# Kernel optimization log

Measured on AMD Instinct MI355X. Metric: run time of the kernel, lower is better.

The kernel has to match this reference:

```python
import jax, jax.numpy as jnp
import numpy as np

B, T, E, H, L = 16, 512, 768, 12, 100
D = E // H
LN_EPS = 1e-12
NEG = -1e9


def setup_inputs() -> dict:
    key = jax.random.key(0)
    ks = jax.random.split(key, 12)
    s = 1.0 / np.sqrt(E)
    inp = {
        "last_hidden_states": jax.random.normal(ks[0], (B, T, E), jnp.float32),
        "att_mask": jnp.ones((B, T), jnp.float32),
        "type_emb": jax.random.normal(ks[1], (L, E), jnp.float32),
        # learned params
        "tp": jax.random.normal(ks[2], (E,), jnp.float32),
        "Wq": jax.random.normal(ks[3], (E, E), jnp.float32) * s,
        "bq": jnp.zeros((E,), jnp.float32),
        "Wk": jax.random.normal(ks[4], (E, E), jnp.float32) * s,
        "bk": jnp.zeros((E,), jnp.float32),
        "Wv": jax.random.normal(ks[5], (E, E), jnp.float32) * s,
        "bv": jnp.zeros((E,), jnp.float32),
        "Wo": jax.random.normal(ks[6], (E, E), jnp.float32) * s,
        "bo": jnp.zeros((E,), jnp.float32),
        "ln_g": jnp.ones((E,), jnp.float32),
        "ln_b": jnp.zeros((E,), jnp.float32),
    }
    return inp


def _layer_norm(x, g, b):
    mu = x.mean(-1, keepdims=True)
    var = ((x - mu) ** 2).mean(-1, keepdims=True)
    return (x - mu) * jax.lax.rsqrt(var + LN_EPS) * g + b


def reference(last_hidden_states, att_mask, type_emb, tp,
              Wq, bq, Wk, bk, Wv, bv, Wo, bo, ln_g, ln_b):
    b, t, e = last_hidden_states.shape
    # --- label cross-attention (no head split, no scaling) ---
    scores = jnp.einsum('bte,le->btl', last_hidden_states, type_emb)      # [b,t,l]
    att = jax.nn.softmax(scores, axis=-1)
    first_label_emb = jnp.einsum('btl,le->bte', att, type_emb)            # [b,t,e]

    h_truth = last_hidden_states + first_label_emb
    h_unknown = last_hidden_states + tp                                   # broadcast tp over [b,t]

    # --- two-stream masked self-attention: Q from unknown, K/V from truth,
    #     each position masked from attending to its own truth state ---
    q = (h_unknown @ Wq + bq).reshape(b, t, H, D)
    k = (h_truth @ Wk + bk).reshape(b, t, H, D)
    v = (h_truth @ Wv + bv).reshape(b, t, H, D)
    logits = jnp.einsum('bqhd,bkhd->bhqk', q, k) / np.sqrt(D).astype(np.float32)
    pad_bias = (1.0 - att_mask)[:, None, None, :] * NEG                   # [b,1,1,t]
    diag_bias = jnp.eye(t, dtype=logits.dtype)[None, None] * NEG          # [1,1,t,t]
    probs = jax.nn.softmax(logits + pad_bias + diag_bias, axis=-1)
    ctx = jnp.einsum('bhqk,bkhd->bqhd', probs, v).reshape(b, t, e)
    attn_out = ctx @ Wo + bo
    twice_hidden = _layer_norm(attn_out + h_unknown, ln_g, ln_b)

    out = twice_hidden + last_hidden_states + first_label_emb
    return out, scores
```

## Files before the change

### kernel.cpp

```cpp
#include <hip/hip_runtime.h>

typedef unsigned char u8;
typedef unsigned short u16;
typedef u16 u16x4 __attribute__((ext_vector_type(4)));
typedef u16 u16x8 __attribute__((ext_vector_type(8)));
typedef __bf16 bf16x8 __attribute__((ext_vector_type(8)));
typedef float f32x2 __attribute__((ext_vector_type(2)));
typedef float f32x4 __attribute__((ext_vector_type(4)));
typedef long longx2 __attribute__((ext_vector_type(2)));

#define BB 16
#define TT 512
#define EE 768
#define HH 12
#define DD 64
#define LL 100
#define BT (BB*TT)
#define BTE ((size_t)BT*EE)
#define LOG2E 1.44269504f
#define QSCALE (0.125f*LOG2E)
#define FIXMAX 44.0f

__device__ __forceinline__ float bf2f(u16 u){
  union { float f; unsigned int i; } v; v.i = ((unsigned int)u) << 16; return v.f;
}
__device__ __forceinline__ u16 f2bf(float f){
  __bf16 h = (__bf16)f;
  union { __bf16 h; u16 u; } v; v.h = h; return v.u;
}
__device__ __forceinline__ u16 pk_fp8(float a, float b){
  return (u16)(__builtin_amdgcn_cvt_pk_fp8_f32(a, b, 0, false) & 0xffff);
}
__device__ __forceinline__ u8 f2fp8(float a){
  return (u8)(__builtin_amdgcn_cvt_pk_fp8_f32(a, 0.f, 0, false) & 0xff);
}

__device__ __forceinline__ void gload16(const void* g, void* l){
  __builtin_amdgcn_global_load_lds(
      (const __attribute__((address_space(1))) void*)g,
      (__attribute__((address_space(3))) void*)l, 16, 0, 0);
}

__global__ __launch_bounds__(256,1) void prep_all_kernel(
    const float* __restrict__ Wq, const float* __restrict__ Wk,
    const float* __restrict__ Wv, const float* __restrict__ Wo,
    u8* __restrict__ WT8,
    const float* __restrict__ TE, u16* __restrict__ TEb, u16* __restrict__ TEt,
    const float* __restrict__ mask, float* __restrict__ MBg)
{
  __shared__ float tile[64][65];
  int bx = blockIdx.x;
  int tid = threadIdx.x;
  if (bx < 576){
    int m  = bx / 144, t = bx % 144;
    int tr = t / 12,  tc = t % 12;
    const float* W = (m==0)?Wq : (m==1)?Wk : (m==2)?Wv : Wo;
    u8* dst = WT8 + (size_t)m * EE * EE;
#pragma unroll
    for (int i=0;i<16;i++){
      int idx = tid + 256*i; int r = idx>>6, c = idx&63;
      tile[r][c] = W[(size_t)(tr*64+r)*EE + tc*64 + c];
    }
    __syncthreads();
#pragma unroll
    for (int i=0;i<8;i++){
      int idx = tid + 256*i;
      int r = idx >> 5, cp = idx & 31;
      u16 pk = pk_fp8(tile[cp*2][r], tile[cp*2+1][r]);
      *(u16*)&dst[(size_t)(tc*64+r)*EE + tr*64 + cp*2] = pk;
    }
  } else if (bx < 960){
    int e = (bx - 576)*2 + (tid >> 7);
    int c = tid & 127;
    u16 v = 0;
    if (c < LL) v = f2bf(TE[(size_t)c*EE + e]);
    TEt[(size_t)e*128 + c] = v;
    if (e < 128){
#pragma unroll
      for (int k=c; k<EE; k+=128)
        TEb[(size_t)e*EE + k] = (e < LL) ? f2bf(TE[(size_t)e*EE + k]) : (u16)0;
    }
  } else {
    int i = (bx - 960)*256 + tid;
    MBg[i] = (1.0f - mask[i]) * (-1e9f * LOG2E) - FIXMAX;
  }
}

__global__ __launch_bounds__(64) void label_scores_kernel(
    const float* __restrict__ X, const u16* __restrict__ TEb,
    float* __restrict__ scores_out, u16* __restrict__ att)
{
  int m0 = blockIdx.x * 16;
  int lane = threadIdx.x;
  int l15 = lane & 15, g = lane >> 4;

  const float* xrow = X + (size_t)(m0 + l15)*EE;
  f32x4 s[7] = {};
  for (int k0=0; k0<EE; k0+=64){
    bf16x8 af[2];
#pragma unroll
    for (int kk=0;kk<2;kk++){
      const float* src = xrow + k0 + kk*32 + g*8;
      float4 a = *(const float4*)src, b = *(const float4*)(src+4);
      bf16x8 o;
      o[0]=(__bf16)a.x; o[1]=(__bf16)a.y; o[2]=(__bf16)a.z; o[3]=(__bf16)a.w;
      o[4]=(__bf16)b.x; o[5]=(__bf16)b.y; o[6]=(__bf16)b.z; o[7]=(__bf16)b.w;
      af[kk] = o;
    }
#pragma unroll
    for (int nt=0;nt<7;nt++){
      bf16x8 b0 = *(const bf16x8*)&TEb[(size_t)(nt*16+l15)*EE + k0 + g*8];
      bf16x8 b1 = *(const bf16x8*)&TEb[(size_t)(nt*16+l15)*EE + k0 + 32 + g*8];
      s[nt] = __builtin_amdgcn_mfma_f32_16x16x32_bf16(af[0], b0, s[nt], 0,0,0);
      s[nt] = __builtin_amdgcn_mfma_f32_16x16x32_bf16(af[1], b1, s[nt], 0,0,0);
    }
  }

  int rowb = m0 + g*4;
#pragma unroll
  for (int nt=0;nt<7;nt++){
    int col = nt*16 + l15;
    if (col < LL){
#pragma unroll
      for (int r=0;r<4;r++)
        scores_out[(size_t)(rowb + r)*LL + col] = s[nt][r];
    }
  }
  if (l15 >= 4){
#pragma unroll
    for (int r=0;r<4;r++) s[6][r] = -1e30f;
  }
  float inv[4];
#pragma unroll
  for (int r=0;r<4;r++){
    float tm = s[0][r];
#pragma unroll
    for (int nt=1;nt<7;nt++) tm = fmaxf(tm, s[nt][r]);
    tm = fmaxf(tm, __shfl_xor(tm, 1, 16));
    tm = fmaxf(tm, __shfl_xor(tm, 2, 16));
    tm = fmaxf(tm, __shfl_xor(tm, 4, 16));
    tm = fmaxf(tm, __shfl_xor(tm, 8, 16));
    float ps = 0.f;
#pragma unroll
    for (int nt=0;nt<7;nt++){
      float p = exp2f((s[nt][r] - tm) * LOG2E);
      s[nt][r] = p; ps += p;
    }
    ps += __shfl_xor(ps, 1, 16);
    ps += __shfl_xor(ps, 2, 16);
    ps += __shfl_xor(ps, 4, 16);
    ps += __shfl_xor(ps, 8, 16);
    inv[r] = 1.f/ps;
  }
#pragma unroll
  for (int nt=0;nt<7;nt++){
    int col = nt*16 + l15;
#pragma unroll
    for (int r=0;r<4;r++)
      att[(size_t)(rowb + r)*128 + col] = f2bf(s[nt][r] * inv[r]);
  }
  {
    int col = 112 + l15;
#pragma unroll
    for (int r=0;r<4;r++) att[(size_t)(rowb + r)*128 + col] = 0;
  }
}

__global__ __launch_bounds__(256,1) void gemm_fle_kernel(
    const u16* __restrict__ A, const u16* __restrict__ BTw,
    const float* __restrict__ Xf, const float* __restrict__ tp,
    u8* __restrict__ HT8, u8* __restrict__ HU8, int N, int K)
{
  __shared__ u16 As[128*40];
  __shared__ u16 Bs[128*40];
  int nb = N >> 7;
  int m0 = (blockIdx.x / nb) << 7;
  int n0 = (blockIdx.x % nb) << 7;
  int tid  = threadIdx.x, lane = tid & 63, w = tid >> 6;
  int wm = (w >> 1) << 6, wn = (w & 1) << 6;
  int lr = lane & 15, lk = (lane >> 4) << 3;

  f32x4 acc[4][4] = {};

  for (int k0 = 0; k0 < K; k0 += 32){
    __syncthreads();
#pragma unroll
    for (int i=0;i<2;i++){
      int idx = tid + (i<<8);
      int row = idx >> 2, kq = (idx & 3) << 3;
      *(u16x8*)&As[row*40 + kq] = *(const u16x8*)&A  [(size_t)(m0+row)*K + k0 + kq];
      *(u16x8*)&Bs[row*40 + kq] = *(const u16x8*)&BTw[(size_t)(n0+row)*K + k0 + kq];
    }
    __syncthreads();
    bf16x8 af[4], bfr[4];
#pragma unroll
    for (int i=0;i<4;i++) af [i] = *(const bf16x8*)&As[(wm + i*16 + lr)*40 + lk];
#pragma unroll
    for (int j=0;j<4;j++) bfr[j] = *(const bf16x8*)&Bs[(wn + j*16 + lr)*40 + lk];
#pragma unroll
    for (int i=0;i<4;i++)
#pragma unroll
      for (int j=0;j<4;j++)
        acc[i][j] = __builtin_amdgcn_mfma_f32_16x16x32_bf16(af[i], bfr[j], acc[i][j], 0, 0, 0);
  }

  int rbase = (lane >> 4) << 2;
#pragma unroll
  for (int j=0;j<4;j++){
    int col = n0 + wn + j*16 + lr;
    float tpv = tp[col];
#pragma unroll
    for (int i=0;i<4;i++){
#pragma unroll
      for (int r=0;r<4;r++){
        int row = m0 + wm + i*16 + rbase + r;
        float x = Xf[(size_t)row*EE + col];
        HT8[(size_t)row*EE + col] = f2fp8(x + acc[i][j][r]);
        HU8[(size_t)row*EE + col] = f2fp8(x + tpv);
      }
    }
  }
}

template<int NB, int FUSED>
__global__ __launch_bounds__(256,2) void gemm8_kernel(
    const u8* __restrict__ A0, const u8* __restrict__ A1,
    const u8* __restrict__ Wb,
    const float* __restrict__ b0, const float* __restrict__ b1,
    const float* __restrict__ b2,
    u16* __restrict__ C0, u16* __restrict__ C1, u16* __restrict__ C2)
{
  __shared__ __align__(16) u8 smem[33792];
  u8* As = smem;
  u8* Bs = smem + 16384;
  u16* Cs = (u16*)smem;
  const int K = EE;

  int nwg = gridDim.x;
  int bid = blockIdx.x;
  int cpx = nwg >> 3;
  int swz = (bid & 7) * cpx + (bid >> 3);
  int mb = swz / NB, nb = swz % NB;
  int m0 = mb << 7;
  int n0 = (FUSED ? (nb % 6) : nb) << 7;

  int which = FUSED ? (nb / 6) : 0;
  const u8* Ap; const u8* Wp; const float* bp; u16* Cp;
  if (!FUSED){ Ap = A0; Wp = Wb; bp = b0; Cp = C0; }
  else {
    if (which == 0){ Ap = A0; Wp = Wb;                      bp = b0; Cp = C0; }
    else if (which == 1){ Ap = A1; Wp = Wb + (size_t)EE*EE; bp = b1; Cp = C1; }
    else { Ap = A1; Wp = Wb + 2*(size_t)EE*EE;              bp = b2; Cp = C2; }
  }

  int tid = threadIdx.x, lane = tid & 63, w = tid >> 6;
  int wm = (w >> 1) << 6, wn = (w & 1) << 6;
  int lr = lane & 15, g = lane >> 4;
  int lrow = lane >> 3;
  int lchunk = (lane & 7) ^ lrow;

  f32x4 acc[4][4] = {};

  for (int k0 = 0; k0 < K; k0 += 128){
    __syncthreads();
#pragma unroll
    for (int t=0;t<4;t++){
      int r0 = w*32 + t*8;
      gload16(&Ap[(size_t)(m0 + r0 + lrow)*K + k0 + (lchunk<<4)], &As[r0*128]);
      gload16(&Wp[(size_t)(n0 + r0 + lrow)*K + k0 + (lchunk<<4)], &Bs[r0*128]);
    }
    __syncthreads();
#pragma unroll
    for (int t=0;t<2;t++){
      int cs = ((t<<2) + g) ^ (lr & 7);
      longx2 af[4], bfr[4];
#pragma unroll
      for (int i=0;i<4;i++) af [i] = *(const longx2*)&As[(wm + i*16 + lr)*128 + (cs<<4)];
#pragma unroll
      for (int j=0;j<4;j++) bfr[j] = *(const longx2*)&Bs[(wn + j*16 + lr)*128 + (cs<<4)];
#pragma unroll
      for (int i=0;i<4;i++)
#pragma unroll
        for (int j=0;j<4;j++){
          acc[i][j] = __builtin_amdgcn_mfma_f32_16x16x32_fp8_fp8(af[i][0], bfr[j][0], acc[i][j], 0, 0, 0);
          acc[i][j] = __builtin_amdgcn_mfma_f32_16x16x32_fp8_fp8(af[i][1], bfr[j][1], acc[i][j], 0, 0, 0);
        }
    }
  }

  int rbase = (lane >> 4) << 2;
  float scq = (FUSED && which==0) ? QSCALE : 1.0f;
  __syncthreads();
#pragma unroll
  for (int j=0;j<4;j++){
    int col = wn + j*16 + lr;
    float bv = bp[n0 + col];
#pragma unroll
    for (int i=0;i<4;i++)
#pragma unroll
      for (int r=0;r<4;r++)
        Cs[(wm + i*16 + rbase + r)*132 + col] = f2bf((acc[i][j][r] + bv) * scq);
  }
  __syncthreads();

  if (FUSED && which == 2){
    int bb = m0 >> 9, t0 = m0 & 511;
    int colb = tid >> 2;
    int tq = (tid & 3) << 3;
#pragma unroll
    for (int c2=0;c2<2;c2++){
      int col = colb + (c2<<6);
      int hh = (n0 + col) >> 6, d = (n0 + col) & 63;
      u16* dst = &Cp[((size_t)(bb*HH + hh)*DD + d)*TT + t0];
#pragma unroll
      for (int s=0;s<4;s++){
        int tt = tq + (s<<5);
        u16x8 v;
#pragma unroll
        for (int e=0;e<8;e++) v[e] = Cs[(tt+e)*132 + col];
        *(u16x8*)&dst[tt] = v;
      }
    }
  } else {
#pragma unroll
    for (int p=0;p<2;p++){
      int row = (tid >> 2) + (p<<6);
      int c0 = (tid & 3) << 3;
      size_t gbase = (size_t)(m0 + row)*EE + n0;
      const u16* src = &Cs[row*132];
#pragma unroll
      for (int s=0;s<4;s++){
        int c = c0 + (s<<5);
        u16x4 lo = *(const u16x4*)&src[c];
        u16x4 hi = *(const u16x4*)&src[c+4];
        u16x8 v;
#pragma unroll
        for (int e=0;e<4;e++){ v[e] = lo[e]; v[e+4] = hi[e]; }
        *(u16x8*)&Cp[gbase + c] = v;
      }
    }
  }
}

__global__ __launch_bounds__(256,3) void attn_mfma_kernel(
    const u16* __restrict__ Q, const u16* __restrict__ K,
    const u16* __restrict__ VT, const float* __restrict__ MBg,
    u8* __restrict__ CTX8)
{
  __shared__ u16 Ks [2][64*64];
  __shared__ u16 VTs[2][64*64];
  __shared__ u16 Pl [4][32*72];

  int bx = blockIdx.x;
  int bh = bx % (BB*HH), q0 = (bx / (BB*HH)) << 7;
  int b = bh / HH, h = bh % HH;
  int tid = threadIdx.x, lane = tid & 63, w = tid >> 6;
  int l15 = lane & 15, g = lane >> 4;
  int wq0 = q0 + w*32;
  size_t rowbase = (size_t)b*TT;
  u16* pw = &Pl[w][0];
  const u16* Kbh = K  + rowbase*EE + h*DD;
  const u16* Vbh = VT + (size_t)bh*DD*TT;
  int lrow = lane >> 3, lchunk = (lane & 7) ^ (lane >> 3);

  bf16x8 qf[2][2];
#pragma unroll
  for (int i=0;i<2;i++)
#pragma unroll
    for (int kk=0;kk<2;kk++)
      qf[i][kk] = *(const bf16x8*)&Q[(rowbase + wq0 + i*16 + l15)*EE + h*DD + kk*32 + g*8];

  f32x4 ctxf[2][4] = {};
  float lrun[2][4] = {};

#define STAGE(buf, k0)                                                          \
  { _Pragma("unroll")                                                           \
    for (int it=0; it<2; ++it){                                                 \
      int r0 = w*16 + it*8;                                                     \
      gload16(&Kbh[(size_t)((k0) + r0 + lrow)*EE + (lchunk<<3)], &Ks [buf][r0*64]); \
      gload16(&Vbh[(size_t)(r0 + lrow)*TT + (k0) + (lchunk<<3)], &VTs[buf][r0*64]); } }

  STAGE(0, 0);

  for (int kt=0; kt<8; ++kt){
    int k0 = kt << 6;
    int buf = kt & 1;
    __syncthreads();

    float mb[4];
#pragma unroll
    for (int kb=0;kb<4;kb++) mb[kb] = MBg[rowbase + k0 + kb*16 + l15];

    if (kt < 7) STAGE(buf^1, k0+64);

    f32x4 s[2][4] = {};
#pragma unroll
    for (int kk=0;kk<2;kk++){
      int cs = ((kk<<2) + g) ^ (l15 & 7);
      bf16x8 kf[4];
#pragma unroll
      for (int kb=0;kb<4;kb++)
        kf[kb] = *(const bf16x8*)&Ks[buf][(kb*16 + l15)*64 + (cs<<3)];
#pragma unroll
      for (int i=0;i<2;i++)
#pragma unroll
        for (int kb=0;kb<4;kb++)
          s[i][kb] = __builtin_amdgcn_mfma_f32_16x16x32_bf16(qf[i][kk], kf[kb], s[i][kb], 0,0,0);
    }

    if ((k0 < wq0 + 32) && (k0 + 64 > wq0)){
#pragma unroll
      for (int i=0;i<2;i++){
        int qr = wq0 + i*16 + g*4;
#pragma unroll
        for (int kb=0;kb<4;kb++){
          int kpos = k0 + kb*16 + l15;
#pragma unroll
          for (int r=0;r<4;r++)
            if (kpos == qr + r) s[i][kb][r] -= 1e9f*LOG2E;
        }
      }
    }

#pragma unroll
    for (int i=0;i<2;i++)
#pragma unroll
      for (int kb=0;kb<4;kb++)
#pragma unroll
        for (int r=0;r<4;r++){
          float p = exp2f(s[i][kb][r] + mb[kb]);
          lrun[i][r] += p;
          pw[(i*16 + g*4 + r)*72 + kb*16 + l15] = f2bf(p);
        }

    bf16x8 pa[2][2];
#pragma unroll
    for (int i=0;i<2;i++)
#pragma unroll
      for (int kk=0;kk<2;kk++)
        pa[i][kk] = *(const bf16x8*)&pw[(i*16 + l15)*72 + kk*32 + g*8];

#pragma unroll
    for (int kk=0;kk<2;kk++){
      int cs = ((kk<<2) + g) ^ (l15 & 7);
      bf16x8 vf[4];
#pragma unroll
      for (int dj=0;dj<4;dj++)
        vf[dj] = *(const bf16x8*)&VTs[buf][(dj*16 + l15)*64 + (cs<<3)];
#pragma unroll
      for (int i=0;i<2;i++)
#pragma unroll
        for (int dj=0;dj<4;dj++)
          ctxf[i][dj] = __builtin_amdgcn_mfma_f32_16x16x32_bf16(pa[i][kk], vf[dj], ctxf[i][dj], 0,0,0);
    }
  }
#undef STAGE

  float inv[2][4];
#pragma unroll
  for (int i=0;i<2;i++)
#pragma unroll
    for (int r=0;r<4;r++){
      float l = lrun[i][r];
      l += __shfl_xor(l, 1, 16);
      l += __shfl_xor(l, 2, 16);
      l += __shfl_xor(l, 4, 16);
      l += __shfl_xor(l, 8, 16);
      inv[i][r] = 1.0f / l;
    }
#pragma unroll
  for (int i=0;i<2;i++)
#pragma unroll
    for (int dj=0;dj<4;dj++)
#pragma unroll
      for (int r=0;r<4;r++)
        pw[(i*16 + g*4 + r)*64 + dj*16 + l15] = f2bf(ctxf[i][dj][r] * inv[i][r]);
#pragma unroll
  for (int t=0;t<4;t++){
    int row = lane >> 1, c = ((lane & 1)<<5) + t*8;
    const u16* pv = &pw[row*64 + c];
    u16x4 o8;
#pragma unroll
    for (int e=0;e<4;e++) o8[e] = pk_fp8(bf2f(pv[2*e]), bf2f(pv[2*e+1]));
    *(u16x4*)&CTX8[(rowbase + wq0 + row)*EE + h*DD + c] = o8;
  }
}

__global__ __launch_bounds__(192,1) void ln_out_kernel(
    const u16* __restrict__ AO, const u8* __restrict__ HU8,
    const u8* __restrict__ HT8, const float* __restrict__ g,
    const float* __restrict__ bta, float* __restrict__ out)
{
  __shared__ float red[3];
  int r = blockIdx.x, tid = threadIdx.x;
  size_t base = (size_t)r*EE;
  int e0 = tid*4;
  u16x4 ao = *(const u16x4*)&AO[base+e0];
  int hu4 = *(const int*)&HU8[base+e0];
  int ht4 = *(const int*)&HT8[base+e0];
  f32x2 hulo = __builtin_amdgcn_cvt_pk_f32_fp8(hu4, false);
  f32x2 huhi = __builtin_amdgcn_cvt_pk_f32_fp8(hu4, true);
  f32x2 htlo = __builtin_amdgcn_cvt_pk_f32_fp8(ht4, false);
  f32x2 hthi = __builtin_amdgcn_cvt_pk_f32_fp8(ht4, true);
  float huv[4] = {hulo[0], hulo[1], huhi[0], huhi[1]};
  float htv[4] = {htlo[0], htlo[1], hthi[0], hthi[1]};
  float x[4];
#pragma unroll
  for (int j=0;j<4;j++) x[j] = bf2f(ao[j]) + huv[j];

  float s = x[0]+x[1]+x[2]+x[3];
#pragma unroll
  for (int o=32;o;o>>=1) s += __shfl_xor(s, o, 64);
  int w = tid>>6;
  if ((tid&63)==0) red[w] = s;
  __syncthreads();
  float mu = (red[0]+red[1]+red[2]) * (1.0f/EE);
  __syncthreads();
  float d2 = 0.f;
#pragma unroll
  for (int j=0;j<4;j++){ float d = x[j]-mu; d2 += d*d; }
#pragma unroll
  for (int o=32;o;o>>=1) d2 += __shfl_xor(d2, o, 64);
  if ((tid&63)==0) red[w] = d2;
  __syncthreads();
  float var = (red[0]+red[1]+red[2]) * (1.0f/EE);
  float rs = rsqrtf(var + 1e-12f);
  float4 gg = *(const float4*)&g[e0];
  float4 bb = *(const float4*)&bta[e0];
  float4 o4;
  o4.x = (x[0]-mu)*rs*gg.x + bb.x + htv[0];
  o4.y = (x[1]-mu)*rs*gg.y + bb.y + htv[1];
  o4.z = (x[2]-mu)*rs*gg.z + bb.z + htv[2];
  o4.w = (x[3]-mu)*rs*gg.w + bb.w + htv[3];
  *(float4*)&out[base+e0] = o4;
}

extern "C" void kernel_launch(void* const* d_in, const int* in_sizes, int n_in,
                              void* d_out, int out_size, void* d_ws, size_t ws_size,
                              hipStream_t stream)
{
  (void)in_sizes; (void)n_in; (void)out_size; (void)ws_size;
  const float* X    = (const float*)d_in[0];
  const float* mask = (const float*)d_in[1];
  const float* TE   = (const float*)d_in[2];
  const float* tp   = (const float*)d_in[3];
  const float* Wq   = (const float*)d_in[4];
  const float* bq   = (const float*)d_in[5];
  const float* Wk   = (const float*)d_in[6];
  const float* bk   = (const float*)d_in[7];
  const float* Wv   = (const float*)d_in[8];
  const float* bv   = (const float*)d_in[9];
  const float* Wo   = (const float*)d_in[10];
  const float* bo   = (const float*)d_in[11];
  const float* ln_g = (const float*)d_in[12];
  const float* ln_b = (const float*)d_in[13];

  float* out    = (float*)d_out;
  float* scores = out + BTE;

  char* p = (char*)d_ws;
  u8*  HT8  = (u8*)p;  p += BTE;
  u8*  HU8  = (u8*)p;  p += BTE;
  u8*  CTX8 = (u8*)p;  p += BTE;
  u8*  WT8  = (u8*)p;  p += (size_t)4*EE*EE;
  u16* Qb   = (u16*)p; p += BTE*2;
  u16* Kb   = (u16*)p; p += BTE*2;
  u16* VTb  = (u16*)p; p += BTE*2;
  u16* AOb  = (u16*)p; p += BTE*2;
  u16* ATT  = (u16*)p; p += (size_t)BT*128*2;
  u16* TEb  = (u16*)p; p += (size_t)128*EE*2;
  u16* TEt  = (u16*)p; p += (size_t)EE*128*2;
  float* MBg = (float*)p;

  prep_all_kernel<<<dim3(992), dim3(256), 0, stream>>>(
      Wq, Wk, Wv, Wo, WT8, TE, TEb, TEt, mask, MBg);

  label_scores_kernel<<<dim3(BT/16), dim3(64), 0, stream>>>(X, TEb, scores, ATT);

  gemm_fle_kernel<<<dim3((BT/128)*(EE/128)), dim3(256), 0, stream>>>(
      ATT, TEt, X, tp, HT8, HU8, EE, 128);

  gemm8_kernel<18,1><<<dim3(64*18), dim3(256), 0, stream>>>(
      HU8, HT8, WT8, bq, bk, bv, Qb, Kb, VTb);

  attn_mfma_kernel<<<dim3(BB*HH*4), dim3(256), 0, stream>>>(Qb, Kb, VTb, MBg, CTX8);

  gemm8_kernel<6,0><<<dim3(64*6), dim3(256), 0, stream>>>(
      CTX8, nullptr, WT8 + 3*(size_t)EE*EE, bo, nullptr, nullptr, AOb, nullptr, nullptr);

  ln_out_kernel<<<dim3(BT), dim3(192), 0, stream>>>(AOb, HU8, HT8, ln_g, ln_b, out);
}
```

Before: 114.7 us.

## Drop K/V double buffering in attention kernel to raise occupancy

Replaces the double-buffered K/V shared-memory staging with a single buffer that is loaded, synchronized, consumed, then synchronized again each iteration. The launch bound goes from 3 to 4 blocks per CU. The P scratch row stride changes from 72 to 76 to alter the LDS bank mapping. This cuts LDS use and register pressure so more waves can hide latency, but it gives up the overlap of the next tile's loads with the current tile's compute and adds a second barrier per iteration.

Result: slower. 141.6 us (+23.5%).

```diff
diff --git a/kernel.cpp b/kernel.cpp
--- a/kernel.cpp
+++ b/kernel.cpp
@@ -20,6 +20,7 @@
 #define LOG2E 1.44269504f
 #define QSCALE (0.125f*LOG2E)
 #define FIXMAX 44.0f
+#define PSTR 76
 
 __device__ __forceinline__ float bf2f(u16 u){
   union { float f; unsigned int i; } v; v.i = ((unsigned int)u) << 16; return v.f;
@@ -342,14 +343,14 @@
   }
 }
 
-__global__ __launch_bounds__(256,3) void attn_mfma_kernel(
+__global__ __launch_bounds__(256,4) void attn_mfma_kernel(
     const u16* __restrict__ Q, const u16* __restrict__ K,
     const u16* __restrict__ VT, const float* __restrict__ MBg,
     u8* __restrict__ CTX8)
 {
-  __shared__ u16 Ks [2][64*64];
-  __shared__ u16 VTs[2][64*64];
-  __shared__ u16 Pl [4][32*72];
+  __shared__ u16 Ks [64*64];
+  __shared__ u16 VTs[64*64];
+  __shared__ u16 Pl [4][32*PSTR];
 
   int bx = blockIdx.x;
   int bh = bx % (BB*HH), q0 = (bx / (BB*HH)) << 7;
@@ -373,25 +374,20 @@
   f32x4 ctxf[2][4] = {};
   float lrun[2][4] = {};
 
-#define STAGE(buf, k0)                                                          \
-  { _Pragma("unroll")                                                           \
-    for (int it=0; it<2; ++it){                                                 \
-      int r0 = w*16 + it*8;                                                     \
-      gload16(&Kbh[(size_t)((k0) + r0 + lrow)*EE + (lchunk<<3)], &Ks [buf][r0*64]); \
-      gload16(&Vbh[(size_t)(r0 + lrow)*TT + (k0) + (lchunk<<3)], &VTs[buf][r0*64]); } }
-
-  STAGE(0, 0);
-
   for (int kt=0; kt<8; ++kt){
     int k0 = kt << 6;
-    int buf = kt & 1;
-    __syncthreads();
 
     float mb[4];
 #pragma unroll
     for (int kb=0;kb<4;kb++) mb[kb] = MBg[rowbase + k0 + kb*16 + l15];
 
-    if (kt < 7) STAGE(buf^1, k0+64);
+#pragma unroll
+    for (int it=0; it<2; ++it){
+      int r0 = w*16 + it*8;
+      gload16(&Kbh[(size_t)(k0 + r0 + lrow)*EE + (lchunk<<3)], &Ks [r0*64]);
+      gload16(&Vbh[(size_t)(r0 + lrow)*TT + k0 + (lchunk<<3)], &VTs[r0*64]);
+    }
+    __syncthreads();
 
     f32x4 s[2][4] = {};
 #pragma unroll
@@ -400,7 +396,7 @@
       bf16x8 kf[4];
 #pragma unroll
       for (int kb=0;kb<4;kb++)
-        kf[kb] = *(const bf16x8*)&Ks[buf][(kb*16 + l15)*64 + (cs<<3)];
+        kf[kb] = *(const bf16x8*)&Ks[(kb*16 + l15)*64 + (cs<<3)];
 #pragma unroll
       for (int i=0;i<2;i++)
 #pragma unroll
@@ -430,7 +426,7 @@
         for (int r=0;r<4;r++){
           float p = exp2f(s[i][kb][r] + mb[kb]);
           lrun[i][r] += p;
-          pw[(i*16 + g*4 + r)*72 + kb*16 + l15] = f2bf(p);
+          pw[(i*16 + g*4 + r)*PSTR + kb*16 + l15] = f2bf(p);
         }
 
     bf16x8 pa[2][2];
@@ -438,7 +434,7 @@
     for (int i=0;i<2;i++)
 #pragma unroll
       for (int kk=0;kk<2;kk++)
-        pa[i][kk] = *(const bf16x8*)&pw[(i*16 + l15)*72 + kk*32 + g*8];
+        pa[i][kk] = *(const bf16x8*)&pw[(i*16 + l15)*PSTR + kk*32 + g*8];
 
 #pragma unroll
     for (int kk=0;kk<2;kk++){
@@ -446,15 +442,15 @@
       bf16x8 vf[4];
 #pragma unroll
       for (int dj=0;dj<4;dj++)
-        vf[dj] = *(const bf16x8*)&VTs[buf][(dj*16 + l15)*64 + (cs<<3)];
+        vf[dj] = *(const bf16x8*)&VTs[(dj*16 + l15)*64 + (cs<<3)];
 #pragma unroll
       for (int i=0;i<2;i++)
 #pragma unroll
         for (int dj=0;dj<4;dj++)
           ctxf[i][dj] = __builtin_amdgcn_mfma_f32_16x16x32_bf16(pa[i][kk], vf[dj], ctxf[i][dj], 0,0,0);
     }
-  }
-#undef STAGE
+    __syncthreads();
+  }
 
   float inv[2][4];
 #pragma unroll
```
